# Performance work log

Hardware: AMD Instinct MI355X
Metric: run time of the kernel (lower is better)

## Reference

```python
import jax, jax.numpy as jnp
import numpy as np

B, N, D = 4, 4096, 128

def setup_inputs() -> dict:
    key = jax.random.key(0)
    k1, k2 = jax.random.split(key)
    x = jax.random.normal(k1, (B, N, D), dtype=jnp.float32)
    a = jax.random.normal(k2, (2 * D, 1), dtype=jnp.float32)
    return {"x": x, "a": a}

def reference(x, a):
    # matmul(cat([x_i, x_j], -1), a) == x_i @ a1 + x_j @ a2, so avoid the
    # O(B*N*N*2D) concat: compute two O(B*N) projections and broadcast-add.
    a1 = a[:D, 0]   # [D]
    a2 = a[D:, 0]   # [D]
    s_i = x @ a1    # [B, N]  (row / source term)
    s_j = x @ a2    # [B, N]  (col / target term)
    e = s_i[:, :, None] + s_j[:, None, :]          # [B, N, N]
    e = jnp.where(e > 0, e, 0.2 * e)               # leaky_relu(0.2)
    attention = jax.nn.softmax(e, axis=-1)         # row softmax
    return attention[..., None]                    # [B, N, N, 1]
```

## Files before the change

### kernel.cpp

```cpp
#include <hip/hip_runtime.h>

#define BB 4
#define NN 4096
#define DD 128
#define RB 8

typedef float vf4 __attribute__((ext_vector_type(4)));

__device__ __forceinline__ float ex2(float x) { return __builtin_amdgcn_exp2f(x); }

__global__ __launch_bounds__(256) void score_kernel(const float* __restrict__ x,
                                                    const float* __restrict__ a,
                                                    float* __restrict__ si_lg,
                                                    float* __restrict__ sj_lg) {
    const float L2E = 1.4426950408889634f;
    int wave = threadIdx.x >> 6;
    int lane = threadIdx.x & 63;
    int row  = blockIdx.x * 4 + wave;
    const float* xr = x + (size_t)row * DD;
    float x0 = xr[lane];
    float x1 = xr[lane + 64];
    float d1 = x0 * a[lane]      + x1 * a[lane + 64];
    float d2 = x0 * a[DD + lane] + x1 * a[DD + lane + 64];
    #pragma unroll
    for (int off = 1; off < 64; off <<= 1) {
        d1 += __shfl_xor(d1, off, 64);
        d2 += __shfl_xor(d2, off, 64);
    }
    if (lane == 0) {
        si_lg[row] = d1 * L2E;
        sj_lg[row] = d2 * L2E;
    }
}

__global__ __launch_bounds__(256) void denom_kernel(const float* __restrict__ si_lg,
                                                    const float* __restrict__ sj_lg,
                                                    float* __restrict__ Mrow) {
    int wave_g = blockIdx.x * 4 + (threadIdx.x >> 6);
    int lane   = threadIdx.x & 63;
    int b      = wave_g >> 10;
    int i0     = (wave_g & 1023) * 4;

    const float* sjb = sj_lg + b * NN;
    vf4 e1[16], e2[16];
    float kmax = -INFINITY;
    #pragma unroll
    for (int g = 0; g < 16; ++g) {
        vf4 s = *reinterpret_cast<const vf4*>(sjb + g * 256 + lane * 4);
        kmax = fmaxf(fmaxf(fmaxf(s.x, s.y), fmaxf(s.z, s.w)), kmax);
        e2[g].x = ex2(0.2f * s.x); e2[g].y = ex2(0.2f * s.y);
        e2[g].z = ex2(0.2f * s.z); e2[g].w = ex2(0.2f * s.w);
        e1[g].x = ex2(s.x); e1[g].y = ex2(s.y);
        e1[g].z = ex2(s.z); e1[g].w = ex2(s.w);
    }
    #pragma unroll
    for (int off = 1; off < 64; off <<= 1)
        kmax = fmaxf(kmax, __shfl_xor(kmax, off, 64));

    #pragma unroll
    for (int r = 0; r < 4; ++r) {
        const int i = i0 + r;
        const float si = si_lg[b * NN + i];
        const float t  = si + kmax;
        const float mr = fmaxf(t, 0.2f * t);
        const float A1 = ex2(si - mr);
        const float A2 = ex2(0.2f * si - mr);
        float sum = 0.f;
        #pragma unroll
        for (int g = 0; g < 16; ++g) {
            sum += fmaxf(A1 * e1[g].x, A2 * e2[g].x)
                 + fmaxf(A1 * e1[g].y, A2 * e2[g].y)
                 + fmaxf(A1 * e1[g].z, A2 * e2[g].z)
                 + fmaxf(A1 * e1[g].w, A2 * e2[g].w);
        }
        #pragma unroll
        for (int off = 1; off < 64; off <<= 1)
            sum += __shfl_xor(sum, off, 64);
        if (lane == 0)
            Mrow[b * NN + i] = mr + __builtin_amdgcn_logf(sum);
    }
}

__global__ __launch_bounds__(256) void stream_kernel(const float* __restrict__ si_lg,
                                                     const float* __restrict__ sj_lg,
                                                     const float* __restrict__ Mrow,
                                                     float* __restrict__ out) {
    const int b    = blockIdx.x >> 9;
    const int i0   = (blockIdx.x & 511) * RB;
    const int wave = threadIdx.x >> 6;
    const int lane = threadIdx.x & 63;

    const float* sjb = sj_lg + b * NN;
    vf4 sv[16];
    #pragma unroll
    for (int g = 0; g < 16; ++g)
        sv[g] = *reinterpret_cast<const vf4*>(sjb + g * 256 + lane * 4);

    #pragma unroll
    for (int r = 0; r < RB / 4; ++r) {
        const int i = i0 + wave * (RB / 4) + r;
        const float si = si_lg[b * NN + i];
        const float M  = Mrow[b * NN + i];
        const float u  = si - M;
        const float v  = 0.2f * si - M;

        float* orow = out + (size_t)(b * NN + i) * NN;
        #pragma unroll
        for (int g = 0; g < 16; ++g) {
            vf4 s = sv[g];
            vf4 o;
            o.x = ex2(fmaxf(u + s.x, fmaf(0.2f, s.x, v)));
            o.y = ex2(fmaxf(u + s.y, fmaf(0.2f, s.y, v)));
            o.z = ex2(fmaxf(u + s.z, fmaf(0.2f, s.z, v)));
            o.w = ex2(fmaxf(u + s.w, fmaf(0.2f, s.w, v)));
            *reinterpret_cast<vf4*>(orow + g * 256 + lane * 4) = o;
        }
    }
}

extern "C" void kernel_launch(void* const* d_in, const int* in_sizes, int n_in,
                              void* d_out, int out_size, void* d_ws, size_t ws_size,
                              hipStream_t stream) {
    const float* x = (const float*)d_in[0];
    const float* a = (const float*)d_in[1];
    float* out = (float*)d_out;
    float* si_lg = (float*)d_ws;
    float* sj_lg = si_lg + BB * NN;
    float* Mrow  = sj_lg + BB * NN;

    score_kernel<<<(BB * NN) / 4, 256, 0, stream>>>(x, a, si_lg, sj_lg);
    denom_kernel<<<1024, 256, 0, stream>>>(si_lg, sj_lg, Mrow);
    stream_kernel<<<(BB * NN) / RB, 256, 0, stream>>>(si_lg, sj_lg, Mrow, out);
}
```

Before: 63.65 us.

## Fuse denominator pass into streaming softmax kernel and use nontemporal stores

Removes the separate denom kernel and its Mrow buffer. Each wave now computes the row max from the sj vector and the row sum of exponentials itself, then writes the normalized outputs. Output stores become nontemporal to avoid polluting cache with the 256MB write stream. This saves a kernel launch and its serialization, at the cost of doing the exponential work twice per element (once for the sum, once for the output) inside the bandwidth-bound kernel.

```diff
diff --git a/kernel.cpp b/kernel.cpp
--- a/kernel.cpp
+++ b/kernel.cpp
@@ -33,58 +33,9 @@
     }
 }
 
-__global__ __launch_bounds__(256) void denom_kernel(const float* __restrict__ si_lg,
-                                                    const float* __restrict__ sj_lg,
-                                                    float* __restrict__ Mrow) {
-    int wave_g = blockIdx.x * 4 + (threadIdx.x >> 6);
-    int lane   = threadIdx.x & 63;
-    int b      = wave_g >> 10;
-    int i0     = (wave_g & 1023) * 4;
-
-    const float* sjb = sj_lg + b * NN;
-    vf4 e1[16], e2[16];
-    float kmax = -INFINITY;
-    #pragma unroll
-    for (int g = 0; g < 16; ++g) {
-        vf4 s = *reinterpret_cast<const vf4*>(sjb + g * 256 + lane * 4);
-        kmax = fmaxf(fmaxf(fmaxf(s.x, s.y), fmaxf(s.z, s.w)), kmax);
-        e2[g].x = ex2(0.2f * s.x); e2[g].y = ex2(0.2f * s.y);
-        e2[g].z = ex2(0.2f * s.z); e2[g].w = ex2(0.2f * s.w);
-        e1[g].x = ex2(s.x); e1[g].y = ex2(s.y);
-        e1[g].z = ex2(s.z); e1[g].w = ex2(s.w);
-    }
-    #pragma unroll
-    for (int off = 1; off < 64; off <<= 1)
-        kmax = fmaxf(kmax, __shfl_xor(kmax, off, 64));
-
-    #pragma unroll
-    for (int r = 0; r < 4; ++r) {
-        const int i = i0 + r;
-        const float si = si_lg[b * NN + i];
-        const float t  = si + kmax;
-        const float mr = fmaxf(t, 0.2f * t);
-        const float A1 = ex2(si - mr);
-        const float A2 = ex2(0.2f * si - mr);
-        float sum = 0.f;
-        #pragma unroll
-        for (int g = 0; g < 16; ++g) {
-            sum += fmaxf(A1 * e1[g].x, A2 * e2[g].x)
-                 + fmaxf(A1 * e1[g].y, A2 * e2[g].y)
-                 + fmaxf(A1 * e1[g].z, A2 * e2[g].z)
-                 + fmaxf(A1 * e1[g].w, A2 * e2[g].w);
-        }
-        #pragma unroll
-        for (int off = 1; off < 64; off <<= 1)
-            sum += __shfl_xor(sum, off, 64);
-        if (lane == 0)
-            Mrow[b * NN + i] = mr + __builtin_amdgcn_logf(sum);
-    }
-}
-
-__global__ __launch_bounds__(256) void stream_kernel(const float* __restrict__ si_lg,
-                                                     const float* __restrict__ sj_lg,
-                                                     const float* __restrict__ Mrow,
-                                                     float* __restrict__ out) {
+__global__ __launch_bounds__(256) void softmax_kernel(const float* __restrict__ si_lg,
+                                                      const float* __restrict__ sj_lg,
+                                                      float* __restrict__ out) {
     const int b    = blockIdx.x >> 9;
     const int i0   = (blockIdx.x & 511) * RB;
     const int wave = threadIdx.x >> 6;
@@ -92,28 +43,52 @@
 
     const float* sjb = sj_lg + b * NN;
     vf4 sv[16];
+    float kmax = -INFINITY;
     #pragma unroll
-    for (int g = 0; g < 16; ++g)
-        sv[g] = *reinterpret_cast<const vf4*>(sjb + g * 256 + lane * 4);
+    for (int g = 0; g < 16; ++g) {
+        vf4 s = *reinterpret_cast<const vf4*>(sjb + g * 256 + lane * 4);
+        sv[g] = s;
+        kmax = fmaxf(fmaxf(fmaxf(s.x, s.y), fmaxf(s.z, s.w)), kmax);
+    }
+    #pragma unroll
+    for (int off = 1; off < 64; off <<= 1)
+        kmax = fmaxf(kmax, __shfl_xor(kmax, off, 64));
 
     #pragma unroll
     for (int r = 0; r < RB / 4; ++r) {
         const int i = i0 + wave * (RB / 4) + r;
         const float si = si_lg[b * NN + i];
-        const float M  = Mrow[b * NN + i];
-        const float u  = si - M;
-        const float v  = 0.2f * si - M;
+        const float c  = si + kmax;
+        const float m  = fmaxf(c, 0.2f * c);
+        const float u  = si - m;
+        const float v  = 0.2f * si - m;
+
+        float lsum = 0.f;
+        #pragma unroll
+        for (int g = 0; g < 16; ++g) {
+            vf4 s = sv[g];
+            lsum += ex2(fmaxf(u + s.x, fmaf(0.2f, s.x, v)))
+                  + ex2(fmaxf(u + s.y, fmaf(0.2f, s.y, v)))
+                  + ex2(fmaxf(u + s.z, fmaf(0.2f, s.z, v)))
+                  + ex2(fmaxf(u + s.w, fmaf(0.2f, s.w, v)));
+        }
+        #pragma unroll
+        for (int off = 1; off < 64; off <<= 1)
+            lsum += __shfl_xor(lsum, off, 64);
+        const float L  = __builtin_amdgcn_logf(lsum);
+        const float u2 = u - L;
+        const float v2 = v - L;
 
         float* orow = out + (size_t)(b * NN + i) * NN;
         #pragma unroll
         for (int g = 0; g < 16; ++g) {
             vf4 s = sv[g];
             vf4 o;
-            o.x = ex2(fmaxf(u + s.x, fmaf(0.2f, s.x, v)));
-            o.y = ex2(fmaxf(u + s.y, fmaf(0.2f, s.y, v)));
-            o.z = ex2(fmaxf(u + s.z, fmaf(0.2f, s.z, v)));
-            o.w = ex2(fmaxf(u + s.w, fmaf(0.2f, s.w, v)));
-            *reinterpret_cast<vf4*>(orow + g * 256 + lane * 4) = o;
+            o.x = ex2(fmaxf(u2 + s.x, fmaf(0.2f, s.x, v2)));
+            o.y = ex2(fmaxf(u2 + s.y, fmaf(0.2f, s.y, v2)));
+            o.z = ex2(fmaxf(u2 + s.z, fmaf(0.2f, s.z, v2)));
+            o.w = ex2(fmaxf(u2 + s.w, fmaf(0.2f, s.w, v2)));
+            __builtin_nontemporal_store(o, reinterpret_cast<vf4*>(orow + g * 256 + lane * 4));
         }
     }
 }
@@ -126,9 +101,7 @@
     float* out = (float*)d_out;
     float* si_lg = (float*)d_ws;
     float* sj_lg = si_lg + BB * NN;
-    float* Mrow  = sj_lg + BB * NN;
 
     score_kernel<<<(BB * NN) / 4, 256, 0, stream>>>(x, a, si_lg, sj_lg);
-    denom_kernel<<<1024, 256, 0, stream>>>(si_lg, sj_lg, Mrow);
-    stream_kernel<<<(BB * NN) / RB, 256, 0, stream>>>(si_lg, sj_lg, Mrow, out);
+    softmax_kernel<<<(BB * NN) / RB, 256, 0, stream>>>(si_lg, sj_lg, out);
 }
```

Measured after the change: 56.73 us. 1.12x faster.
